# Optimization experiments

Hardware: AMD Instinct MI355X
Metric: run time of the kernel (lower is better)

Reference implementation:

```python
import jax, jax.numpy as jnp
import numpy as np

PAD = 99          # padding sentinel in y_true, per tf.not_equal(y_true, 99)
NEG = -1e9        # safe -inf surrogate (avoids nan grads from true -inf)


def _ctc_loss(log_probs, labels, label_len, blank):
    """Per-example CTC negative log-likelihood (forward algorithm in log space).

    log_probs: [B, T, C] log-softmax outputs
    labels:    [B, L] int labels (values < blank for valid positions)
    label_len: [B] number of valid labels per example
    """
    B, T, C = log_probs.shape
    L = labels.shape[1]
    S = 2 * L + 1  # extended label seq: blank, y1, blank, ..., yL, blank

    ext = jnp.full((B, S), blank, dtype=jnp.int32).at[:, 1::2].set(labels.astype(jnp.int32))
    # skip transition s-2 -> s allowed only for label positions whose label differs from the previous one
    ext_m2 = jnp.pad(ext[:, :-2], ((0, 0), (2, 0)), constant_values=blank)
    skip = (jnp.arange(S)[None, :] % 2 == 1) & (ext != ext_m2)  # [B, S]

    # per-time log prob of each extended symbol: [B, T, S] -> time-major [T, B, S]
    lp = jnp.take_along_axis(log_probs, ext[:, None, :], axis=2)
    lp = jnp.transpose(lp, (1, 0, 2))

    alpha0 = jnp.full((B, S), NEG, dtype=log_probs.dtype)
    alpha0 = alpha0.at[:, 0].set(lp[0, :, 0])
    alpha0 = alpha0.at[:, 1].set(jnp.where(label_len > 0, lp[0, :, 1], NEG))

    def step(alpha, lp_t):
        s1 = jnp.pad(alpha[:, :-1], ((0, 0), (1, 0)), constant_values=NEG)
        s2 = jnp.pad(alpha[:, :-2], ((0, 0), (2, 0)), constant_values=NEG)
        a = jnp.logaddexp(alpha, s1)
        a = jnp.where(skip, jnp.logaddexp(a, s2), a)
        return a + lp_t, None

    alphaT, _ = jax.lax.scan(step, alpha0, lp[1:])

    idx_last = (2 * label_len).astype(jnp.int32)  # trailing blank position
    a_blank = jnp.take_along_axis(alphaT, idx_last[:, None], axis=1)[:, 0]
    a_label = jnp.take_along_axis(alphaT, jnp.maximum(idx_last - 1, 0)[:, None], axis=1)[:, 0]
    a_label = jnp.where(label_len > 0, a_label, NEG)
    return -jnp.logaddexp(a_blank, a_label)  # [B]


def setup_inputs() -> dict:
    key = jax.random.key(0)
    k1, k2 = jax.random.split(key)
    y_true = jax.random.randint(k1, (1024, 32), 0, 99, dtype=jnp.int32)
    y_pred = jax.random.normal(k2, (1024, 256, 128), dtype=jnp.float32)
    return {"y_true": y_true, "y_pred": y_pred}


def reference(y_true, y_pred):
    C = y_pred.shape[-1]
    blank = C - 1  # blank_index=-1 in tf.nn.ctc_loss
    label_len = jnp.sum(y_true != PAD, axis=1).astype(jnp.int32)
    log_probs = jax.nn.log_softmax(y_pred, axis=-1)
    loss = _ctc_loss(log_probs, y_true, label_len, blank)
    return jnp.mean(loss)
```

## Files before the change

### kernel.cpp

```cpp
#include <hip/hip_runtime.h>
#include <hip/hip_fp16.h>

#define B_    1024
#define T_    256
#define C_    128
#define LMAX  32
#define DUMP  33
#define RSTR  36
#define GSTR  (T_ * RSTR)

__device__ __forceinline__ float readlanef(float v, int l) {
    return __int_as_float(__builtin_amdgcn_readlane(__float_as_int(v), l));
}
__device__ __forceinline__ float readlane0f(float v) {
    return __int_as_float(__builtin_amdgcn_readfirstlane(__float_as_int(v)));
}
template<int CTRL>
__device__ __forceinline__ float dpp0f(float v) {
    return __int_as_float(__builtin_amdgcn_update_dpp(0, __float_as_int(v),
                                                      CTRL, 0xF, 0xF, true));
}
template<int CTRL>
__device__ __forceinline__ int dpp0i(int v) {
    return __builtin_amdgcn_update_dpp(0, v, CTRL, 0xF, 0xF, true);
}
__device__ __forceinline__ float halfsum_dpp(float v) {
    v += dpp0f<0x111>(v); v += dpp0f<0x112>(v);
    v += dpp0f<0x114>(v); v += dpp0f<0x118>(v);
    v += dpp0f<0x142>(v);
    return v;
}
__device__ __forceinline__ float halfsum_shfl(float v) {
    #pragma unroll
    for (int off = 16; off; off >>= 1) v += __shfl_xor(v, off);
    return v;
}
__device__ __forceinline__ float wavesum_dpp(float v) {
    v += dpp0f<0x111>(v); v += dpp0f<0x112>(v); v += dpp0f<0x114>(v);
    v += dpp0f<0x118>(v); v += dpp0f<0x142>(v); v += dpp0f<0x143>(v);
    return readlanef(v, 63);
}
__device__ __forceinline__ float wavemax_dpp(float v) {
    v = fmaxf(v, dpp0f<0x111>(v)); v = fmaxf(v, dpp0f<0x112>(v));
    v = fmaxf(v, dpp0f<0x114>(v)); v = fmaxf(v, dpp0f<0x118>(v));
    v = fmaxf(v, dpp0f<0x142>(v)); v = fmaxf(v, dpp0f<0x143>(v));
    return readlanef(v, 63);
}

template<bool DPP>
__device__ __forceinline__ void fstepL(float& a, float& a64, float p,
                                       int lane, bool skip) {
    float am1, am2;
    if constexpr (DPP) { am1 = dpp0f<0x138>(a); am2 = dpp0f<0x138>(am1); }
    else {
        float s1 = __shfl_up(a, 1), s2 = __shfl_up(a, 2);
        am1 = (lane < 1) ? 0.f : s1;
        am2 = (lane < 2) ? 0.f : s2;
    }
    float a63 = readlanef(a, 63);
    float pb  = readlane0f(p);
    float sum = a + am1 + (skip ? am2 : 0.f);
    a64 = (a64 + a63) * pb;
    a   = sum * p;
}
template<bool DPP>
__device__ __forceinline__ void bstepL(float& B, float& b64, float p,
                                       int lane, bool skipT, bool l63) {
    float r1, b2;
    if constexpr (DPP) { r1 = dpp0f<0x130>(B); b2 = dpp0f<0x130>(r1); }
    else {
        float s1 = __shfl_down(B, 1), s2 = __shfl_down(B, 2);
        r1 = (lane < 63) ? s1 : 0.f;
        b2 = (lane < 62) ? s2 : 0.f;
    }
    float bs1 = l63 ? b64 : r1;
    float pb  = readlane0f(p);
    float sum = B + bs1 + (skipT ? b2 : 0.f);
    b64 = b64 * pb;
    B   = sum * p;
}
template<bool DPP>
__device__ __forceinline__ void rescaleL(float& x, float& x64, float& logZ) {
    float m;
    if constexpr (DPP) m = wavemax_dpp(x);
    else {
        float v = x;
        #pragma unroll
        for (int off = 32; off; off >>= 1) v = fmaxf(v, __shfl_xor(v, off));
        m = v;
    }
    m = fmaxf(fmaxf(m, x64), 1e-30f);
    float r = __builtin_amdgcn_rcpf(m);
    x *= r; x64 *= r; logZ += __logf(m);
}

#define LOAD16F(dst, tb) { _Pragma("unroll")                                   \
    for (int j = 0; j < 16; ++j)                                               \
        dst[j] = __half2float(gp[(size_t)((tb) + j) * RSTR]); }

template<bool DPP>
__device__ __forceinline__ void fwd_half(const __half* gp, int lane, bool skip,
                                         int L, float& a_o, float& a64_o, float& lz_o) {
    float xA[16], xB[16];
    LOAD16F(xA, 0); LOAD16F(xB, 16);
    float a = (lane == 0 || (lane == 1 && L > 0)) ? xA[0] : 0.f;
    float a64 = 0.f, logZ = 0.f;
    #pragma unroll
    for (int k = 1; k < 8; ++k) fstepL<DPP>(a, a64, xA[k], lane, skip);
    rescaleL<DPP>(a, a64, logZ);
    #pragma unroll
    for (int k = 8; k < 16; ++k) fstepL<DPP>(a, a64, xA[k], lane, skip);
    rescaleL<DPP>(a, a64, logZ);
    for (int c = 1; c <= 5; c += 2) {
        LOAD16F(xA, (c + 1) * 16);
        #pragma unroll
        for (int k = 0; k < 8; ++k) fstepL<DPP>(a, a64, xB[k], lane, skip);
        rescaleL<DPP>(a, a64, logZ);
        #pragma unroll
        for (int k = 8; k < 16; ++k) fstepL<DPP>(a, a64, xB[k], lane, skip);
        rescaleL<DPP>(a, a64, logZ);
        LOAD16F(xB, (c + 2) * 16);
        #pragma unroll
        for (int k = 0; k < 8; ++k) fstepL<DPP>(a, a64, xA[k], lane, skip);
        rescaleL<DPP>(a, a64, logZ);
        #pragma unroll
        for (int k = 8; k < 16; ++k) fstepL<DPP>(a, a64, xA[k], lane, skip);
        rescaleL<DPP>(a, a64, logZ);
    }
    #pragma unroll
    for (int k = 0; k < 8; ++k) fstepL<DPP>(a, a64, xB[k], lane, skip);
    rescaleL<DPP>(a, a64, logZ);
    #pragma unroll
    for (int k = 8; k < 16; ++k) fstepL<DPP>(a, a64, xB[k], lane, skip);
    rescaleL<DPP>(a, a64, logZ);
    a_o = a; a64_o = a64; lz_o = logZ;
}
template<bool DPP>
__device__ __forceinline__ void bwd_half(const __half* gp, int lane, bool skipT,
                                         int L, float& B_o, float& b64_o, float& lz_o) {
    bool l63 = (lane == 63);
    float xA[16], xB[16];
    LOAD16F(xA, 240); LOAD16F(xB, 224);
    int twoL = 2 * L;
    float p255 = xA[15];
    float B   = ((lane == twoL) || (L > 0 && lane == twoL - 1)) ? p255 : 0.f;
    float b64 = (twoL == 64) ? readlane0f(p255) : 0.f;
    float logZ = 0.f;
    #pragma unroll
    for (int k = 1; k < 8; ++k) bstepL<DPP>(B, b64, xA[15 - k], lane, skipT, l63);
    rescaleL<DPP>(B, b64, logZ);
    #pragma unroll
    for (int k = 8; k < 16; ++k) bstepL<DPP>(B, b64, xA[15 - k], lane, skipT, l63);
    rescaleL<DPP>(B, b64, logZ);
    for (int c = 1; c <= 5; c += 2) {
        LOAD16F(xA, 240 - (c + 1) * 16);
        #pragma unroll
        for (int k = 0; k < 8; ++k) bstepL<DPP>(B, b64, xB[15 - k], lane, skipT, l63);
        rescaleL<DPP>(B, b64, logZ);
        #pragma unroll
        for (int k = 8; k < 16; ++k) bstepL<DPP>(B, b64, xB[15 - k], lane, skipT, l63);
        rescaleL<DPP>(B, b64, logZ);
        LOAD16F(xB, 240 - (c + 2) * 16);
        #pragma unroll
        for (int k = 0; k < 8; ++k) bstepL<DPP>(B, b64, xA[15 - k], lane, skipT, l63);
        rescaleL<DPP>(B, b64, logZ);
        #pragma unroll
        for (int k = 8; k < 16; ++k) bstepL<DPP>(B, b64, xA[15 - k], lane, skipT, l63);
        rescaleL<DPP>(B, b64, logZ);
    }
    #pragma unroll
    for (int k = 0; k < 8; ++k) bstepL<DPP>(B, b64, xB[15 - k], lane, skipT, l63);
    rescaleL<DPP>(B, b64, logZ);
    #pragma unroll
    for (int k = 8; k < 16; ++k) bstepL<DPP>(B, b64, xB[15 - k], lane, skipT, l63);
    rescaleL<DPP>(B, b64, logZ);
    B_o = B; b64_o = b64; lz_o = logZ;
}

__global__ void __launch_bounds__(512) prob_kernel(const float* __restrict__ yp,
                                                   const int* __restrict__ yt,
                                                   __half* __restrict__ g) {
    __shared__ int firstOwner[128];
    int tid  = threadIdx.x;
    int w    = tid >> 6;
    int lane = tid & 63;
    int li   = lane & 31;
    int b    = blockIdx.x;

    if (tid < 128) firstOwner[tid] = DUMP;
    float ptst = halfsum_dpp((float)(lane + 1));
    bool sumok = __all(readlanef(ptst, 31) == 528.0f &&
                       readlanef(ptst, 63) == 1552.0f) != 0;
    __syncthreads();
    if (tid < 33) {
        int c = (tid == 0) ? (C_ - 1)
                           : min(max(yt[b * LMAX + tid - 1], 0), C_ - 1);
        atomicMin(&firstOwner[c], tid);
    }
    __syncthreads();
    int s0 = firstOwner[4 * li + 0];
    int s1 = firstOwner[4 * li + 1];
    int s2 = firstOwner[4 * li + 2];
    int s3 = firstOwner[4 * li + 3];

    const float4* srcQ = (const float4*)(yp + ((size_t)b * T_ + w * 32) * C_);
    __half* gb_ = g + (size_t)b * GSTR;
    int rbase = w * 32 + (lane >> 5);

    #define PROC(V, I, HS) {                                                   \
        float e0 = __expf(fminf((V).x, 80.f)), e1 = __expf(fminf((V).y, 80.f));\
        float e2 = __expf(fminf((V).z, 80.f)), e3 = __expf(fminf((V).w, 80.f));\
        float tt = HS(e0 + e1 + e2 + e3);                                      \
        float ss = (lane < 32) ? readlanef(tt, 31) : readlanef(tt, 63);        \
        float rinv = __builtin_amdgcn_rcpf(ss);                                \
        size_t R = (size_t)(rbase + 2 * (I)) * RSTR;                           \
        if (s0 != DUMP) gb_[R + s0] = __float2half_rn(e0 * rinv);              \
        if (s1 != DUMP) gb_[R + s1] = __float2half_rn(e1 * rinv);              \
        if (s2 != DUMP) gb_[R + s2] = __float2half_rn(e2 * rinv);              \
        if (s3 != DUMP) gb_[R + s3] = __float2half_rn(e3 * rinv); }
    #define LOOP(HS) {                                                         \
        float4 u0 = srcQ[lane], u1 = srcQ[64 + lane],                          \
               u2 = srcQ[128 + lane], u3 = srcQ[192 + lane];                   \
        _Pragma("unroll")                                                      \
        for (int ii = 0; ii < 4; ++ii) {                                       \
            float4 n0, n1, n2, n3;                                             \
            if (ii < 3) {                                                      \
                n0 = srcQ[(ii * 4 + 4) * 64 + lane];                           \
                n1 = srcQ[(ii * 4 + 5) * 64 + lane];                           \
                n2 = srcQ[(ii * 4 + 6) * 64 + lane];                           \
                n3 = srcQ[(ii * 4 + 7) * 64 + lane];                           \
            }                                                                  \
            PROC(u0, ii * 4 + 0, HS); PROC(u1, ii * 4 + 1, HS);                \
            PROC(u2, ii * 4 + 2, HS); PROC(u3, ii * 4 + 3, HS);                \
            if (ii < 3) { u0 = n0; u1 = n1; u2 = n2; u3 = n3; }                \
        } }

    if (sumok) LOOP(halfsum_dpp)
    else       LOOP(halfsum_shfl)
    #undef LOOP
    #undef PROC
}

__global__ void __launch_bounds__(128) ctc_kernel(const __half* __restrict__ g,
                                                  const int* __restrict__ yt,
                                                  float* __restrict__ loss) {
    __shared__ int   firstOwner[128];
    __shared__ int   owner[33];
    __shared__ float alphaS[65], BS[66];
    __shared__ float lzA, lzB;
    int tid  = threadIdx.x;
    int w    = tid >> 6;
    int lane = tid & 63;
    int b    = blockIdx.x;
    const int* lab = yt + b * LMAX;

    if (tid < 128) firstOwner[tid] = DUMP;
    int pr = dpp0i<0x138>(lane + 1);
    bool shrok = __all(pr == ((lane == 0) ? 0 : lane)) != 0;
    int pl = dpp0i<0x130>(lane + 1);
    bool shlok = __all(pl == ((lane == 63) ? 0 : lane + 2)) != 0;
    float fs = wavesum_dpp((float)(lane + 1));
    bool fullok = __all(fs == 2080.0f) != 0;
    __syncthreads();
    if (tid < 33) {
        int c = (tid == 0) ? (C_ - 1)
                           : min(max(lab[tid - 1], 0), C_ - 1);
        atomicMin(&firstOwner[c], tid);
    }
    __syncthreads();
    if (tid < 33) {
        int c = (tid == 0) ? (C_ - 1)
                           : min(max(lab[tid - 1], 0), C_ - 1);
        owner[tid] = firstOwner[c];
    }
    __syncthreads();

    int myl = (lane < LMAX) ? lab[lane] : 99;
    unsigned long long bal = __ballot(lane < LMAX && myl != 99);
    int L = __popcll(bal);
    int  j2  = lane >> 1;
    bool odd = (lane & 1) != 0;
    int  myslot = odd ? (1 + j2) : 0;
    const __half* gp = g + (size_t)b * GSTR + owner[myslot];

    if (w == 0) {
        bool skip = odd && (lab[j2] != ((j2 > 0) ? lab[j2 - 1] : (C_ - 1)));
        float a, a64, lz;
        if (shrok && fullok) fwd_half<true >(gp, lane, skip, L, a, a64, lz);
        else                 fwd_half<false>(gp, lane, skip, L, a, a64, lz);
        alphaS[lane] = a;
        if (lane == 0) { alphaS[64] = a64; lzA = lz; }
    } else {
        bool skipT = odd && (lane <= 61) && (lab[min(j2 + 1, 31)] != lab[j2]);
        float Bv, b64, lz;
        if (shlok && fullok) bwd_half<true >(gp, lane, skipT, L, Bv, b64, lz);
        else                 bwd_half<false>(gp, lane, skipT, L, Bv, b64, lz);
        BS[lane] = Bv;
        if (lane == 0) { BS[64] = b64; BS[65] = 0.f; lzB = lz; }
    }
    __syncthreads();
    if (w != 0) return;

    bool skipT = odd && (lane <= 61) && (lab[min(j2 + 1, 31)] != lab[j2]);
    float bex = BS[lane] + BS[lane + 1] + (skipT ? BS[lane + 2] : 0.f);
    float contrib = alphaS[lane] * bex;
    if (lane == 0) contrib += alphaS[64] * BS[64];
    #pragma unroll
    for (int off = 32; off; off >>= 1) contrib += __shfl_xor(contrib, off);
    if (lane == 0) loss[b] = -(__logf(fmaxf(contrib, 1e-37f)) + lzA + lzB);
}

__global__ void __launch_bounds__(256) reduce_kernel(const float* __restrict__ loss,
                                                     float* __restrict__ out) {
    __shared__ float ps[4];
    int t = threadIdx.x;
    float4 v = ((const float4*)loss)[t];
    float s = v.x + v.y + v.z + v.w;
    #pragma unroll
    for (int off = 32; off; off >>= 1) s += __shfl_xor(s, off);
    if ((t & 63) == 0) ps[t >> 6] = s;
    __syncthreads();
    if (t == 0) out[0] = (ps[0] + ps[1] + ps[2] + ps[3]) * (1.0f / B_);
}

extern "C" void kernel_launch(void* const* d_in, const int* in_sizes, int n_in,
                              void* d_out, int out_size, void* d_ws, size_t ws_size,
                              hipStream_t stream) {
    const int*   yt  = (const int*)d_in[0];
    const float* yp  = (const float*)d_in[1];
    float*       out = (float*)d_out;

    size_t gbytes = (size_t)B_ * GSTR * sizeof(__half);
    __half* g    = (__half*)d_ws;
    float*  loss = (float*)((char*)d_ws + gbytes);

    prob_kernel<<<B_, 512, 0, stream>>>(yp, yt, g);
    ctc_kernel<<<B_, 128, 0, stream>>>(g, yt, loss);
    reduce_kernel<<<1, 256, 0, stream>>>(loss, out);
}
```

Baseline: 45.41 us.

## Fuse probability and CTC kernels, keeping per-symbol probabilities in shared memory

Merges the softmax/gather kernel and the forward-backward CTC kernel into one 512-thread block per example. The gathered half-precision probabilities stay in an LDS buffer instead of a global workspace, which removes the global write and re-read and one kernel launch. The cost is that 6 of the 8 waves sit idle during the serial alpha/beta recursion, and the larger LDS footprint (about 18KB) may limit how many blocks share a CU.

```diff
diff --git a/kernel.cpp b/kernel.cpp
--- a/kernel.cpp
+++ b/kernel.cpp
@@ -7,7 +7,6 @@
 #define LMAX  32
 #define DUMP  33
 #define RSTR  36
-#define GSTR  (T_ * RSTR)
 
 __device__ __forceinline__ float readlanef(float v, int l) {
     return __int_as_float(__builtin_amdgcn_readlane(__float_as_int(v), l));
@@ -96,7 +95,7 @@
 
 #define LOAD16F(dst, tb) { _Pragma("unroll")                                   \
     for (int j = 0; j < 16; ++j)                                               \
-        dst[j] = __half2float(gp[(size_t)((tb) + j) * RSTR]); }
+        dst[j] = __half2float(gp[(tb + j) * RSTR]); }
 
 template<bool DPP>
 __device__ __forceinline__ void fwd_half(const __half* gp, int lane, bool skip,
@@ -177,34 +176,50 @@
     B_o = B; b64_o = b64; lz_o = logZ;
 }
 
-__global__ void __launch_bounds__(512) prob_kernel(const float* __restrict__ yp,
-                                                   const int* __restrict__ yt,
-                                                   __half* __restrict__ g) {
-    __shared__ int firstOwner[128];
+__global__ void __launch_bounds__(512) fused_kernel(const float* __restrict__ yp,
+                                                    const int* __restrict__ yt,
+                                                    float* __restrict__ loss) {
+    __shared__ __half lph[T_ * RSTR];
+    __shared__ int    firstOwner[128];
+    __shared__ int    owner[33];
+    __shared__ float  alphaS[65], BS[66];
+    __shared__ float  lzA, lzB;
+
     int tid  = threadIdx.x;
     int w    = tid >> 6;
     int lane = tid & 63;
     int li   = lane & 31;
     int b    = blockIdx.x;
+    const int* lab = yt + b * LMAX;
 
     if (tid < 128) firstOwner[tid] = DUMP;
+
     float ptst = halfsum_dpp((float)(lane + 1));
     bool sumok = __all(readlanef(ptst, 31) == 528.0f &&
                        readlanef(ptst, 63) == 1552.0f) != 0;
+    int pr = dpp0i<0x138>(lane + 1);
+    bool shrok = __all(pr == ((lane == 0) ? 0 : lane)) != 0;
+    int pl = dpp0i<0x130>(lane + 1);
+    bool shlok = __all(pl == ((lane == 63) ? 0 : lane + 2)) != 0;
+    float fsv = wavesum_dpp((float)(lane + 1));
+    bool fullok = __all(fsv == 2080.0f) != 0;
+
     __syncthreads();
     if (tid < 33) {
-        int c = (tid == 0) ? (C_ - 1)
-                           : min(max(yt[b * LMAX + tid - 1], 0), C_ - 1);
+        int c = (tid == 0) ? (C_ - 1) : min(max(lab[tid - 1], 0), C_ - 1);
         atomicMin(&firstOwner[c], tid);
     }
     __syncthreads();
+    if (tid < 33) {
+        int c = (tid == 0) ? (C_ - 1) : min(max(lab[tid - 1], 0), C_ - 1);
+        owner[tid] = firstOwner[c];
+    }
     int s0 = firstOwner[4 * li + 0];
     int s1 = firstOwner[4 * li + 1];
     int s2 = firstOwner[4 * li + 2];
     int s3 = firstOwner[4 * li + 3];
 
     const float4* srcQ = (const float4*)(yp + ((size_t)b * T_ + w * 32) * C_);
-    __half* gb_ = g + (size_t)b * GSTR;
     int rbase = w * 32 + (lane >> 5);
 
     #define PROC(V, I, HS) {                                                   \
@@ -213,11 +228,11 @@
         float tt = HS(e0 + e1 + e2 + e3);                                      \
         float ss = (lane < 32) ? readlanef(tt, 31) : readlanef(tt, 63);        \
         float rinv = __builtin_amdgcn_rcpf(ss);                                \
-        size_t R = (size_t)(rbase + 2 * (I)) * RSTR;                           \
-        if (s0 != DUMP) gb_[R + s0] = __float2half_rn(e0 * rinv);              \
-        if (s1 != DUMP) gb_[R + s1] = __float2half_rn(e1 * rinv);              \
-        if (s2 != DUMP) gb_[R + s2] = __float2half_rn(e2 * rinv);              \
-        if (s3 != DUMP) gb_[R + s3] = __float2half_rn(e3 * rinv); }
+        int R = (rbase + 2 * (I)) * RSTR;                                      \
+        if (s0 != DUMP) lph[R + s0] = __float2half_rn(e0 * rinv);              \
+        if (s1 != DUMP) lph[R + s1] = __float2half_rn(e1 * rinv);              \
+        if (s2 != DUMP) lph[R + s2] = __float2half_rn(e2 * rinv);              \
+        if (s3 != DUMP) lph[R + s3] = __float2half_rn(e3 * rinv); }
     #define LOOP(HS) {                                                         \
         float4 u0 = srcQ[lane], u1 = srcQ[64 + lane],                          \
                u2 = srcQ[128 + lane], u3 = srcQ[192 + lane];                   \
@@ -239,40 +254,7 @@
     else       LOOP(halfsum_shfl)
     #undef LOOP
     #undef PROC
-}
-
-__global__ void __launch_bounds__(128) ctc_kernel(const __half* __restrict__ g,
-                                                  const int* __restrict__ yt,
-                                                  float* __restrict__ loss) {
-    __shared__ int   firstOwner[128];
-    __shared__ int   owner[33];
-    __shared__ float alphaS[65], BS[66];
-    __shared__ float lzA, lzB;
-    int tid  = threadIdx.x;
-    int w    = tid >> 6;
-    int lane = tid & 63;
-    int b    = blockIdx.x;
-    const int* lab = yt + b * LMAX;
-
-    if (tid < 128) firstOwner[tid] = DUMP;
-    int pr = dpp0i<0x138>(lane + 1);
-    bool shrok = __all(pr == ((lane == 0) ? 0 : lane)) != 0;
-    int pl = dpp0i<0x130>(lane + 1);
-    bool shlok = __all(pl == ((lane == 63) ? 0 : lane + 2)) != 0;
-    float fs = wavesum_dpp((float)(lane + 1));
-    bool fullok = __all(fs == 2080.0f) != 0;
-    __syncthreads();
-    if (tid < 33) {
-        int c = (tid == 0) ? (C_ - 1)
-                           : min(max(lab[tid - 1], 0), C_ - 1);
-        atomicMin(&firstOwner[c], tid);
-    }
-    __syncthreads();
-    if (tid < 33) {
-        int c = (tid == 0) ? (C_ - 1)
-                           : min(max(lab[tid - 1], 0), C_ - 1);
-        owner[tid] = firstOwner[c];
-    }
+
     __syncthreads();
 
     int myl = (lane < LMAX) ? lab[lane] : 99;
@@ -281,16 +263,17 @@
     int  j2  = lane >> 1;
     bool odd = (lane & 1) != 0;
     int  myslot = odd ? (1 + j2) : 0;
-    const __half* gp = g + (size_t)b * GSTR + owner[myslot];
 
     if (w == 0) {
+        const __half* gp = &lph[owner[myslot]];
         bool skip = odd && (lab[j2] != ((j2 > 0) ? lab[j2 - 1] : (C_ - 1)));
         float a, a64, lz;
         if (shrok && fullok) fwd_half<true >(gp, lane, skip, L, a, a64, lz);
         else                 fwd_half<false>(gp, lane, skip, L, a, a64, lz);
         alphaS[lane] = a;
         if (lane == 0) { alphaS[64] = a64; lzA = lz; }
-    } else {
+    } else if (w == 1) {
+        const __half* gp = &lph[owner[myslot]];
         bool skipT = odd && (lane <= 61) && (lab[min(j2 + 1, 31)] != lab[j2]);
         float Bv, b64, lz;
         if (shlok && fullok) bwd_half<true >(gp, lane, skipT, L, Bv, b64, lz);
@@ -299,15 +282,16 @@
         if (lane == 0) { BS[64] = b64; BS[65] = 0.f; lzB = lz; }
     }
     __syncthreads();
-    if (w != 0) return;
-
-    bool skipT = odd && (lane <= 61) && (lab[min(j2 + 1, 31)] != lab[j2]);
-    float bex = BS[lane] + BS[lane + 1] + (skipT ? BS[lane + 2] : 0.f);
-    float contrib = alphaS[lane] * bex;
-    if (lane == 0) contrib += alphaS[64] * BS[64];
-    #pragma unroll
-    for (int off = 32; off; off >>= 1) contrib += __shfl_xor(contrib, off);
-    if (lane == 0) loss[b] = -(__logf(fmaxf(contrib, 1e-37f)) + lzA + lzB);
+
+    if (w == 0) {
+        bool skipT = odd && (lane <= 61) && (lab[min(j2 + 1, 31)] != lab[j2]);
+        float bex = BS[lane] + BS[lane + 1] + (skipT ? BS[lane + 2] : 0.f);
+        float contrib = alphaS[lane] * bex;
+        if (lane == 0) contrib += alphaS[64] * BS[64];
+        #pragma unroll
+        for (int off = 32; off; off >>= 1) contrib += __shfl_xor(contrib, off);
+        if (lane == 0) loss[b] = -(__logf(fmaxf(contrib, 1e-37f)) + lzA + lzB);
+    }
 }
 
 __global__ void __launch_bounds__(256) reduce_kernel(const float* __restrict__ loss,
@@ -329,12 +313,8 @@
     const int*   yt  = (const int*)d_in[0];
     const float* yp  = (const float*)d_in[1];
     float*       out = (float*)d_out;
-
-    size_t gbytes = (size_t)B_ * GSTR * sizeof(__half);
-    __half* g    = (__half*)d_ws;
-    float*  loss = (float*)((char*)d_ws + gbytes);
-
-    prob_kernel<<<B_, 512, 0, stream>>>(yp, yt, g);
-    ctc_kernel<<<B_, 128, 0, stream>>>(g, yt, loss);
+    float*       loss = (float*)d_ws;
+
+    fused_kernel<<<B_, 512, 0, stream>>>(yp, yt, loss);
     reduce_kernel<<<1, 256, 0, stream>>>(loss, out);
 }
```

Measured after the change: 42.04 us. 1.08x faster.
